# Kernel tuning notes

Hardware: AMD Instinct MI355X
Metric: run time of the kernel (lower is better)

## Reference

```python
import jax, jax.numpy as jnp
import numpy as np

N, E = 100000, 600000
DIN, DEMB, DOUT = 128, 128, 2
EPS = 1e-5


def setup_inputs() -> dict:
    key = jax.random.key(0)
    ks = jax.random.split(key, 20)
    s = 1.0 / np.sqrt(DIN)
    se = 1.0 / np.sqrt(DEMB)
    inp = {
        'x': jax.random.normal(ks[0], (N, DIN), jnp.float32),
        'edge_index': jax.random.randint(ks[1], (2, E), 0, N, jnp.int64),
        # SAGEConv layer 0 (in->emb): lin_l (with bias) on aggregated, lin_r (no bias) on root
        'Wl0': jax.random.uniform(ks[2], (DIN, DEMB), jnp.float32, -s, s),
        'bl0': jax.random.uniform(ks[3], (DEMB,), jnp.float32, -s, s),
        'Wr0': jax.random.uniform(ks[4], (DIN, DEMB), jnp.float32, -s, s),
        # SAGEConv layer 1 (emb->emb)
        'Wl1': jax.random.uniform(ks[5], (DEMB, DEMB), jnp.float32, -se, se),
        'bl1': jax.random.uniform(ks[6], (DEMB,), jnp.float32, -se, se),
        'Wr1': jax.random.uniform(ks[7], (DEMB, DEMB), jnp.float32, -se, se),
        # BatchNorm affine params (2 BN layers used)
        'g0': jnp.ones((DEMB,), jnp.float32),
        'be0': jnp.zeros((DEMB,), jnp.float32),
        'g1': jnp.ones((DEMB,), jnp.float32),
        'be1': jnp.zeros((DEMB,), jnp.float32),
        # MLP head
        'W1': jax.random.uniform(ks[8], (DEMB, DEMB), jnp.float32, -se, se),
        'b1': jax.random.uniform(ks[9], (DEMB,), jnp.float32, -se, se),
        'W2': jax.random.uniform(ks[10], (DEMB, DEMB), jnp.float32, -se, se),
        'b2': jax.random.uniform(ks[11], (DEMB,), jnp.float32, -se, se),
        'W3': jax.random.uniform(ks[12], (DEMB, DOUT), jnp.float32, -se, se),
        'b3': jax.random.uniform(ks[13], (DOUT,), jnp.float32, -se, se),
    }
    return inp


def _sage_conv(x, edge_index, Wl, bl, Wr):
    # sum-aggregate source features into destination nodes, then transform
    src, dst = edge_index[0], edge_index[1]
    agg = jax.ops.segment_sum(x[src], dst, num_segments=x.shape[0])  # [N, d]
    return agg @ Wl + bl + x @ Wr


def _bn_relu(h, gamma, beta):
    mu = jnp.mean(h, axis=0)
    var = jnp.var(h, axis=0)
    return jax.nn.relu((h - mu) * jax.lax.rsqrt(var + EPS) * gamma + beta)


def reference(x, edge_index, Wl0, bl0, Wr0, Wl1, bl1, Wr1,
              g0, be0, g1, be1, W1, b1, W2, b2, W3, b3):
    # NOTE: original forward zips num_layers convs with num_layers-1 batch_norms,
    # so only the first num_layers-1 = 2 conv blocks execute.
    h = _bn_relu(_sage_conv(x, edge_index, Wl0, bl0, Wr0), g0, be0)
    h = _bn_relu(_sage_conv(h, edge_index, Wl1, bl1, Wr1), g1, be1)
    # dropout p=0.2 is identity in inference mode
    h = jax.nn.relu(h @ W1 + b1)
    h = jax.nn.relu(h @ W2 + b2)
    return h @ W3 + b3
```

## Files before the change

### kernel.cpp

```cpp
#include <hip/hip_runtime.h>

#define EPS 1e-5f

typedef __attribute__((ext_vector_type(8))) short bf16x8;
typedef __attribute__((ext_vector_type(4))) float f32x4;

static __device__ __forceinline__ void split4(float4 f, ushort4& hi, ushort4& lo) {
    float v[4] = {f.x, f.y, f.z, f.w};
    ushort h[4], l[4];
#pragma unroll
    for (int i = 0; i < 4; ++i) {
        unsigned u = __float_as_uint(v[i]);
        h[i] = (ushort)(u >> 16);
        float r = v[i] - __uint_as_float(u & 0xffff0000u);
        l[i] = (ushort)(__float_as_uint(r) >> 16);
    }
    hi = make_ushort4(h[0], h[1], h[2], h[3]);
    lo = make_ushort4(l[0], l[1], l[2], l[3]);
}

static __device__ __forceinline__ float4 bnrelu4(float4 v, float4 a, float4 d) {
    float4 r;
    r.x = fmaxf(a.x * v.x + d.x, 0.f);
    r.y = fmaxf(a.y * v.y + d.y, 0.f);
    r.z = fmaxf(a.z * v.z + d.z, 0.f);
    r.w = fmaxf(a.w * v.w + d.w, 0.f);
    return r;
}

__global__ __launch_bounds__(256) void hist_kernel(
    const int* __restrict__ ei, int* __restrict__ deg, int E)
{
    int e = blockIdx.x * 256 + threadIdx.x;
    if (e >= E) return;
    atomicAdd(&deg[ei[E + e]], 1);
}

__global__ __launch_bounds__(256) void blocksum_kernel(
    const int* __restrict__ deg, int* __restrict__ bsum, int N)
{
    int i = blockIdx.x * 256 + threadIdx.x;
    int v = (i < N) ? deg[i] : 0;
#pragma unroll
    for (int o = 1; o < 64; o <<= 1) v += __shfl_xor(v, o);
    __shared__ int s[4];
    if ((threadIdx.x & 63) == 0) s[threadIdx.x >> 6] = v;
    __syncthreads();
    if (threadIdx.x == 0) bsum[blockIdx.x] = s[0] + s[1] + s[2] + s[3];
}

__global__ __launch_bounds__(512) void scanb_kernel(int* bsum, int NB)
{
    __shared__ int sh[512];
    int t = threadIdx.x;
    int v = (t < NB) ? bsum[t] : 0;
    sh[t] = v;
    __syncthreads();
    for (int o = 1; o < 512; o <<= 1) {
        int add = (t >= o) ? sh[t - o] : 0;
        __syncthreads();
        sh[t] += add;
        __syncthreads();
    }
    if (t < NB) bsum[t] = (t == 0) ? 0 : sh[t - 1];
}

__global__ __launch_bounds__(256) void scanfinal_kernel(
    const int* __restrict__ deg, const int* __restrict__ bsum,
    int* __restrict__ rowptr, int* __restrict__ cursor, int N)
{
    int b = blockIdx.x, t = threadIdx.x;
    int i = b * 256 + t;
    int v = (i < N) ? deg[i] : 0;
    __shared__ int sh[256];
    sh[t] = v;
    __syncthreads();
    for (int o = 1; o < 256; o <<= 1) {
        int add = (t >= o) ? sh[t - o] : 0;
        __syncthreads();
        sh[t] += add;
        __syncthreads();
    }
    int excl = sh[t] - v;
    if (i < N) {
        int rp = bsum[b] + excl;
        rowptr[i] = rp;
        cursor[i] = rp;
        if (i == N - 1) rowptr[N] = rp + v;
    }
}

__global__ __launch_bounds__(256) void fill_kernel(
    const int* __restrict__ ei, int* __restrict__ cursor, int* __restrict__ col, int E)
{
    int e = blockIdx.x * 256 + threadIdx.x;
    if (e >= E) return;
    int d = ei[E + e];
    int pos = atomicAdd(&cursor[d], 1);
    col[pos] = ei[e];
}

template<int BN>
__global__ __launch_bounds__(256) void gather_kernel(
    const float* __restrict__ feat, float* __restrict__ agg,
    const int* __restrict__ rowptr, const int* __restrict__ colIdx,
    const float* __restrict__ bnst, int N)
{
    int gid = blockIdx.x * 256 + threadIdx.x;
    int n = gid >> 5;
    if (n >= N) return;
    int l = gid & 31;
    float4 a4, d4;
    if (BN) {
        a4 = *(const float4*)(bnst + 256 + l * 4);
        d4 = *(const float4*)(bnst + 384 + l * 4);
    }
    int beg = rowptr[n], end = rowptr[n + 1];
    float ax = 0.f, ay = 0.f, az = 0.f, aw = 0.f;
    float bx = 0.f, by = 0.f, bz = 0.f, bw = 0.f;
    int e = beg;
    for (; e + 2 <= end; e += 2) {
        int s0 = colIdx[e], s1 = colIdx[e + 1];
        float4 v0 = *(const float4*)(feat + (size_t)s0 * 128 + l * 4);
        float4 v1 = *(const float4*)(feat + (size_t)s1 * 128 + l * 4);
        if (BN) { v0 = bnrelu4(v0, a4, d4); v1 = bnrelu4(v1, a4, d4); }
        ax += v0.x; ay += v0.y; az += v0.z; aw += v0.w;
        bx += v1.x; by += v1.y; bz += v1.z; bw += v1.w;
    }
    if (e < end) {
        int s0 = colIdx[e];
        float4 v0 = *(const float4*)(feat + (size_t)s0 * 128 + l * 4);
        if (BN) v0 = bnrelu4(v0, a4, d4);
        ax += v0.x; ay += v0.y; az += v0.z; aw += v0.w;
    }
    *(float4*)(agg + (size_t)n * 128 + l * 4) =
        make_float4(ax + bx, ay + by, az + bz, aw + bw);
}

__global__ __launch_bounds__(256) void prepack_kernel(
    const float* __restrict__ W0, const float* __restrict__ W1,
    const float* __restrict__ W2, const float* __restrict__ W3,
    const float* __restrict__ W4, const float* __restrict__ W5,
    ushort* __restrict__ wPk)
{
    int m = blockIdx.y;
    const float* W = (m == 0) ? W0 : (m == 1) ? W1 : (m == 2) ? W2
                   : (m == 3) ? W3 : (m == 4) ? W4 : W5;
    int base = m * 32768;
#pragma unroll
    for (int t = 0; t < 8; ++t) {
        int idx = blockIdx.x * 2048 + t * 256 + threadIdx.x;
        int j = idx & 7, l = (idx >> 3) & 63, cf = (idx >> 9) & 7, kb = idx >> 12;
        int k = kb * 32 + (l >> 4) * 8 + j;
        int n = cf * 16 + (l & 15);
        float v = W[k * 128 + n];
        unsigned u = __float_as_uint(v);
        wPk[base + idx] = (ushort)(u >> 16);
        float r = v - __uint_as_float(u & 0xffff0000u);
        wPk[base + 16384 + idx] = (ushort)(__float_as_uint(r) >> 16);
    }
}

template<int DUAL, int RELU, int STATS, int BN>
__global__ __launch_bounds__(512, 2) void plin_kernel(
    const float* __restrict__ Xa, const float* __restrict__ Xb,
    const ushort* __restrict__ wPair, const float* __restrict__ bias,
    const float* __restrict__ bnst, float* __restrict__ Y,
    float* __restrict__ stOut, int nrows)
{
    __shared__ ushort ldsA[(DUAL ? 2 : 1) * 2 * 2176];
    const int tid  = threadIdx.x;
    const int lane = tid & 63;
    const int w    = tid >> 6;
    const int q = lane >> 4, s = lane & 15;

    constexpr int NM = DUAL + 1;
    bf16x8 wf[NM][4][2];
#pragma unroll
    for (int m = 0; m < NM; ++m)
#pragma unroll
        for (int kb = 0; kb < 4; ++kb) {
            size_t o = (size_t)m * 32768 + (size_t)kb * 4096 + w * 512 + lane * 8;
            wf[m][kb][0] = *(const bf16x8*)(wPair + o);
            wf[m][kb][1] = *(const bf16x8*)(wPair + o + 16384);
        }

    const int srow  = tid >> 5;
    const int sunit = tid & 31;
    float4 bna, bnd;
    if (BN) {
        bna = *(const float4*)(bnst + 256 + sunit * 4);
        bnd = *(const float4*)(bnst + 384 + sunit * 4);
    }

    const int colc = w * 16 + s;
    const float bv = bias[colc];
    float cs = 0.f, cq = 0.f;

    const int NT = (nrows + 15) >> 4;
    const int stride = (int)gridDim.x;
    const int t0 = blockIdx.x;
    const int woff = srow * 136 + sunit * 4;

    if (t0 < NT) {
        int row = t0 * 16 + srow; if (row > nrows - 1) row = nrows - 1;
        float4 va = *(const float4*)(Xa + (size_t)row * 128 + sunit * 4);
        float4 vb;
        if (DUAL) vb = *(const float4*)(Xb + (size_t)row * 128 + sunit * 4);
        if (BN) { if (DUAL) vb = bnrelu4(vb, bna, bnd); else va = bnrelu4(va, bna, bnd); }
        ushort4 h, l;
        split4(va, h, l);
        *(ushort4*)(ldsA + woff)        = h;
        *(ushort4*)(ldsA + 2176 + woff) = l;
        if (DUAL) {
            split4(vb, h, l);
            *(ushort4*)(ldsA + 4352 + woff) = h;
            *(ushort4*)(ldsA + 6528 + woff) = l;
        }
    }

    for (int t = t0; t < NT; t += stride) {
        int tn = t + stride;
        float4 na, nb;
        if (tn < NT) {
            int row = tn * 16 + srow; if (row > nrows - 1) row = nrows - 1;
            na = *(const float4*)(Xa + (size_t)row * 128 + sunit * 4);
            if (DUAL) nb = *(const float4*)(Xb + (size_t)row * 128 + sunit * 4);
        }
        __syncthreads();

        f32x4 acc = (f32x4){0.f, 0.f, 0.f, 0.f};
#pragma unroll
        for (int m = 0; m < NM; ++m) {
            const ushort* pm = ldsA + m * 4352 + s * 136;
#pragma unroll
            for (int kb = 0; kb < 4; ++kb) {
                bf16x8 ah = *(const bf16x8*)(pm + (kb * 4 + q) * 8);
                bf16x8 al = *(const bf16x8*)(pm + 2176 + (kb * 4 + q) * 8);
                acc = __builtin_amdgcn_mfma_f32_16x16x32_bf16(ah, wf[m][kb][0], acc, 0, 0, 0);
                acc = __builtin_amdgcn_mfma_f32_16x16x32_bf16(al, wf[m][kb][0], acc, 0, 0, 0);
                acc = __builtin_amdgcn_mfma_f32_16x16x32_bf16(ah, wf[m][kb][1], acc, 0, 0, 0);
            }
        }

        int r0 = t * 16 + q * 4;
#pragma unroll
        for (int i = 0; i < 4; ++i) {
            int r = r0 + i;
            if (r < nrows) {
                float y = acc[i] + bv;
                if (RELU) y = fmaxf(y, 0.f);
                Y[(size_t)r * 128 + colc] = y;
                if (STATS) { cs += y; cq += y * y; }
            }
        }
        __syncthreads();
        if (tn < NT) {
            if (BN) { if (DUAL) nb = bnrelu4(nb, bna, bnd); else na = bnrelu4(na, bna, bnd); }
            ushort4 h, l;
            split4(na, h, l);
            *(ushort4*)(ldsA + woff)        = h;
            *(ushort4*)(ldsA + 2176 + woff) = l;
            if (DUAL) {
                split4(nb, h, l);
                *(ushort4*)(ldsA + 4352 + woff) = h;
                *(ushort4*)(ldsA + 6528 + woff) = l;
            }
        }
    }

    if (STATS) {
        cs += __shfl_xor(cs, 16); cs += __shfl_xor(cs, 32);
        cq += __shfl_xor(cq, 16); cq += __shfl_xor(cq, 32);
        if (q == 0) {
            atomicAdd(&stOut[colc], cs);
            atomicAdd(&stOut[128 + colc], cq);
        }
    }
}

__global__ void finalize_kernel(float* st, const float* __restrict__ g,
                                const float* __restrict__ be, float inv_n)
{
    int c = threadIdx.x;
    float mu = st[c] * inv_n;
    float var = st[128 + c] * inv_n - mu * mu;
    float rs = rsqrtf(var + EPS);
    float a = g[c] * rs;
    st[256 + c] = a;
    st[384 + c] = be[c] - mu * a;
}

__global__ __launch_bounds__(256) void linout_kernel(
    const float* __restrict__ X, const float* __restrict__ W, const float* __restrict__ b,
    float* __restrict__ out, int nrows)
{
    int r = blockIdx.x * 256 + threadIdx.x;
    if (r >= nrows) return;
    float a0 = 0.f, a1 = 0.f;
    const float* xr = X + (size_t)r * 128;
#pragma unroll 8
    for (int k = 0; k < 128; k += 4) {
        float4 x = *(const float4*)(xr + k);
        a0 += x.x * W[(k + 0) * 2]     + x.y * W[(k + 1) * 2]
            + x.z * W[(k + 2) * 2]     + x.w * W[(k + 3) * 2];
        a1 += x.x * W[(k + 0) * 2 + 1] + x.y * W[(k + 1) * 2 + 1]
            + x.z * W[(k + 2) * 2 + 1] + x.w * W[(k + 3) * 2 + 1];
    }
    float2 o = make_float2(a0 + b[0], a1 + b[1]);
    *(float2*)(out + (size_t)r * 2) = o;
}

extern "C" void kernel_launch(void* const* d_in, const int* in_sizes, int n_in,
                              void* d_out, int out_size, void* d_ws, size_t ws_size,
                              hipStream_t stream) {
    const float* x   = (const float*)d_in[0];
    const int*   ei  = (const int*)d_in[1];
    const float* Wl0 = (const float*)d_in[2];
    const float* bl0 = (const float*)d_in[3];
    const float* Wr0 = (const float*)d_in[4];
    const float* Wl1 = (const float*)d_in[5];
    const float* bl1 = (const float*)d_in[6];
    const float* Wr1 = (const float*)d_in[7];
    const float* g0  = (const float*)d_in[8];
    const float* be0 = (const float*)d_in[9];
    const float* g1  = (const float*)d_in[10];
    const float* be1 = (const float*)d_in[11];
    const float* W1  = (const float*)d_in[12];
    const float* b1  = (const float*)d_in[13];
    const float* W2  = (const float*)d_in[14];
    const float* b2  = (const float*)d_in[15];
    const float* W3  = (const float*)d_in[16];
    const float* b3  = (const float*)d_in[17];
    float* out = (float*)d_out;

    const int N = in_sizes[0] / 128;
    const int E = in_sizes[1] / 2;

    float* A   = (float*)d_ws;
    float* B   = A + (size_t)N * 128;
    float* st0 = B + (size_t)N * 128;
    float* st1 = st0 + 512;
    ushort* wPk = (ushort*)(st1 + 512);
    int* deg    = (int*)(wPk + 6 * 32768);
    int* rowptr = deg + N;
    int* cursor = rowptr + N + 1;
    int* col    = cursor + N;
    int* bsum   = col + E;

    const int edgeGrid   = (E + 255) / 256;
    const int nodeGrid   = (N + 255) / 256;
    const int gatherGrid = ((size_t)N * 32 + 255) / 256;
    const float inv_n = 1.0f / (float)N;

    prepack_kernel<<<dim3(8, 6), 256, 0, stream>>>(Wl0, Wr0, Wl1, Wr1, W1, W2, wPk);

    hipMemsetAsync(deg, 0, (size_t)N * sizeof(int), stream);
    hist_kernel<<<edgeGrid, 256, 0, stream>>>(ei, deg, E);
    blocksum_kernel<<<nodeGrid, 256, 0, stream>>>(deg, bsum, N);
    scanb_kernel<<<1, 512, 0, stream>>>(bsum, nodeGrid);
    scanfinal_kernel<<<nodeGrid, 256, 0, stream>>>(deg, bsum, rowptr, cursor, N);
    fill_kernel<<<edgeGrid, 256, 0, stream>>>(ei, cursor, col, E);

    gather_kernel<0><<<gatherGrid, 256, 0, stream>>>(x, A, rowptr, col, nullptr, N);
    hipMemsetAsync(st0, 0, 256 * sizeof(float), stream);
    plin_kernel<1, 0, 1, 0><<<512, 512, 0, stream>>>(
        A, x, wPk, bl0, nullptr, A, st0, N);
    finalize_kernel<<<1, 128, 0, stream>>>(st0, g0, be0, inv_n);

    gather_kernel<1><<<gatherGrid, 256, 0, stream>>>(A, B, rowptr, col, st0, N);
    hipMemsetAsync(st1, 0, 256 * sizeof(float), stream);
    plin_kernel<1, 0, 1, 1><<<512, 512, 0, stream>>>(
        B, A, wPk + 2 * 32768, bl1, st0, B, st1, N);
    finalize_kernel<<<1, 128, 0, stream>>>(st1, g1, be1, inv_n);

    plin_kernel<0, 1, 0, 1><<<512, 512, 0, stream>>>(
        B, nullptr, wPk + 4 * 32768, b1, st1, A, nullptr, N);
    plin_kernel<0, 1, 0, 0><<<512, 512, 0, stream>>>(
        A, nullptr, wPk + 5 * 32768, b2, nullptr, B, nullptr, N);
    linout_kernel<<<(N + 255) / 256, 256, 0, stream>>>(B, W3, b3, out, N);
}
```

Before: 299.3 us.

## Fuse neighbor gather into SAGE linear kernels and fuse MLP head into one kernel

The separate gather kernels are removed. Each SAGE layer now aggregates neighbor rows inside the MFMA linear kernel while staging a tile, so the aggregated matrix is never written to or read back from global memory. The three MLP-head layers (two 128x128 GEMMs plus the 128->2 output) become one kernel that keeps intermediates in LDS, which removes two full N x 128 round trips and two launches. In exchange, the irregular gather now sits on the GEMM kernel's critical path: it runs synchronously between tiles, and prefetch overlap is lost because the next tile is staged only after the barrier. Occupancy is fixed at 512 blocks of 512 threads.

```diff
diff --git a/kernel.cpp b/kernel.cpp
--- a/kernel.cpp
+++ b/kernel.cpp
@@ -98,43 +98,6 @@
     int d = ei[E + e];
     int pos = atomicAdd(&cursor[d], 1);
     col[pos] = ei[e];
-}
-
-template<int BN>
-__global__ __launch_bounds__(256) void gather_kernel(
-    const float* __restrict__ feat, float* __restrict__ agg,
-    const int* __restrict__ rowptr, const int* __restrict__ colIdx,
-    const float* __restrict__ bnst, int N)
-{
-    int gid = blockIdx.x * 256 + threadIdx.x;
-    int n = gid >> 5;
-    if (n >= N) return;
-    int l = gid & 31;
-    float4 a4, d4;
-    if (BN) {
-        a4 = *(const float4*)(bnst + 256 + l * 4);
-        d4 = *(const float4*)(bnst + 384 + l * 4);
-    }
-    int beg = rowptr[n], end = rowptr[n + 1];
-    float ax = 0.f, ay = 0.f, az = 0.f, aw = 0.f;
-    float bx = 0.f, by = 0.f, bz = 0.f, bw = 0.f;
-    int e = beg;
-    for (; e + 2 <= end; e += 2) {
-        int s0 = colIdx[e], s1 = colIdx[e + 1];
-        float4 v0 = *(const float4*)(feat + (size_t)s0 * 128 + l * 4);
-        float4 v1 = *(const float4*)(feat + (size_t)s1 * 128 + l * 4);
-        if (BN) { v0 = bnrelu4(v0, a4, d4); v1 = bnrelu4(v1, a4, d4); }
-        ax += v0.x; ay += v0.y; az += v0.z; aw += v0.w;
-        bx += v1.x; by += v1.y; bz += v1.z; bw += v1.w;
-    }
-    if (e < end) {
-        int s0 = colIdx[e];
-        float4 v0 = *(const float4*)(feat + (size_t)s0 * 128 + l * 4);
-        if (BN) v0 = bnrelu4(v0, a4, d4);
-        ax += v0.x; ay += v0.y; az += v0.z; aw += v0.w;
-    }
-    *(float4*)(agg + (size_t)n * 128 + l * 4) =
-        make_float4(ax + bx, ay + by, az + bz, aw + bw);
 }
 
 __global__ __launch_bounds__(256) void prepack_kernel(
@@ -161,23 +124,22 @@
     }
 }
 
-template<int DUAL, int RELU, int STATS, int BN>
-__global__ __launch_bounds__(512, 2) void plin_kernel(
-    const float* __restrict__ Xa, const float* __restrict__ Xb,
-    const ushort* __restrict__ wPair, const float* __restrict__ bias,
-    const float* __restrict__ bnst, float* __restrict__ Y,
-    float* __restrict__ stOut, int nrows)
-{
-    __shared__ ushort ldsA[(DUAL ? 2 : 1) * 2 * 2176];
+template<int BN>
+__global__ __launch_bounds__(512, 2) void glin_kernel(
+    const float* __restrict__ X, const int* __restrict__ rowptr,
+    const int* __restrict__ colIdx, const ushort* __restrict__ wPair,
+    const float* __restrict__ bias, const float* __restrict__ bnst,
+    float* __restrict__ Y, float* __restrict__ stOut, int nrows)
+{
+    __shared__ ushort ldsA[2 * 2 * 2176];
     const int tid  = threadIdx.x;
     const int lane = tid & 63;
     const int w    = tid >> 6;
     const int q = lane >> 4, s = lane & 15;
 
-    constexpr int NM = DUAL + 1;
-    bf16x8 wf[NM][4][2];
-#pragma unroll
-    for (int m = 0; m < NM; ++m)
+    bf16x8 wf[2][4][2];
+#pragma unroll
+    for (int m = 0; m < 2; ++m)
 #pragma unroll
         for (int kb = 0; kb < 4; ++kb) {
             size_t o = (size_t)m * 32768 + (size_t)kb * 4096 + w * 512 + lane * 8;
@@ -202,36 +164,46 @@
     const int t0 = blockIdx.x;
     const int woff = srow * 136 + sunit * 4;
 
-    if (t0 < NT) {
-        int row = t0 * 16 + srow; if (row > nrows - 1) row = nrows - 1;
-        float4 va = *(const float4*)(Xa + (size_t)row * 128 + sunit * 4);
-        float4 vb;
-        if (DUAL) vb = *(const float4*)(Xb + (size_t)row * 128 + sunit * 4);
-        if (BN) { if (DUAL) vb = bnrelu4(vb, bna, bnd); else va = bnrelu4(va, bna, bnd); }
+    auto stage = [&](int t) {
+        int row = t * 16 + srow; if (row > nrows - 1) row = nrows - 1;
+        float4 root = *(const float4*)(X + (size_t)row * 128 + sunit * 4);
+        int beg = rowptr[row], end = rowptr[row + 1];
+        float ax = 0.f, ay = 0.f, az = 0.f, aw = 0.f;
+        float bx = 0.f, by = 0.f, bz = 0.f, bw = 0.f;
+        int e = beg;
+        for (; e + 2 <= end; e += 2) {
+            int s0 = colIdx[e], s1 = colIdx[e + 1];
+            float4 v0 = *(const float4*)(X + (size_t)s0 * 128 + sunit * 4);
+            float4 v1 = *(const float4*)(X + (size_t)s1 * 128 + sunit * 4);
+            if (BN) { v0 = bnrelu4(v0, bna, bnd); v1 = bnrelu4(v1, bna, bnd); }
+            ax += v0.x; ay += v0.y; az += v0.z; aw += v0.w;
+            bx += v1.x; by += v1.y; bz += v1.z; bw += v1.w;
+        }
+        if (e < end) {
+            int s0 = colIdx[e];
+            float4 v0 = *(const float4*)(X + (size_t)s0 * 128 + sunit * 4);
+            if (BN) v0 = bnrelu4(v0, bna, bnd);
+            ax += v0.x; ay += v0.y; az += v0.z; aw += v0.w;
+        }
+        float4 agg = make_float4(ax + bx, ay + by, az + bz, aw + bw);
+        if (BN) root = bnrelu4(root, bna, bnd);
         ushort4 h, l;
-        split4(va, h, l);
+        split4(agg, h, l);
         *(ushort4*)(ldsA + woff)        = h;
         *(ushort4*)(ldsA + 2176 + woff) = l;
-        if (DUAL) {
-            split4(vb, h, l);
-            *(ushort4*)(ldsA + 4352 + woff) = h;
-            *(ushort4*)(ldsA + 6528 + woff) = l;
-        }
-    }
+        split4(root, h, l);
+        *(ushort4*)(ldsA + 4352 + woff) = h;
+        *(ushort4*)(ldsA + 6528 + woff) = l;
+    };
+
+    if (t0 < NT) stage(t0);
 
     for (int t = t0; t < NT; t += stride) {
-        int tn = t + stride;
-        float4 na, nb;
-        if (tn < NT) {
-            int row = tn * 16 + srow; if (row > nrows - 1) row = nrows - 1;
-            na = *(const float4*)(Xa + (size_t)row * 128 + sunit * 4);
-            if (DUAL) nb = *(const float4*)(Xb + (size_t)row * 128 + sunit * 4);
-        }
         __syncthreads();
 
         f32x4 acc = (f32x4){0.f, 0.f, 0.f, 0.f};
 #pragma unroll
-        for (int m = 0; m < NM; ++m) {
+        for (int m = 0; m < 2; ++m) {
             const ushort* pm = ldsA + m * 4352 + s * 136;
 #pragma unroll
             for (int kb = 0; kb < 4; ++kb) {
@@ -249,33 +221,134 @@
             int r = r0 + i;
             if (r < nrows) {
                 float y = acc[i] + bv;
-                if (RELU) y = fmaxf(y, 0.f);
                 Y[(size_t)r * 128 + colc] = y;
-                if (STATS) { cs += y; cq += y * y; }
+                cs += y; cq += y * y;
             }
         }
         __syncthreads();
-        if (tn < NT) {
-            if (BN) { if (DUAL) nb = bnrelu4(nb, bna, bnd); else na = bnrelu4(na, bna, bnd); }
+        int tn = t + stride;
+        if (tn < NT) stage(tn);
+    }
+
+    cs += __shfl_xor(cs, 16); cs += __shfl_xor(cs, 32);
+    cq += __shfl_xor(cq, 16); cq += __shfl_xor(cq, 32);
+    if (q == 0) {
+        atomicAdd(&stOut[colc], cs);
+        atomicAdd(&stOut[128 + colc], cq);
+    }
+}
+
+__global__ __launch_bounds__(512, 2) void mlp_kernel(
+    const float* __restrict__ X, const ushort* __restrict__ w1Pk,
+    const ushort* __restrict__ w2Pk, const float* __restrict__ b1,
+    const float* __restrict__ b2, const float* __restrict__ W3,
+    const float* __restrict__ b3, const float* __restrict__ bnst,
+    float* __restrict__ out, int nrows)
+{
+    __shared__ ushort ldsP[2 * 2176];
+    __shared__ float  ldsY[16 * 132];
+    const int tid  = threadIdx.x;
+    const int lane = tid & 63;
+    const int w    = tid >> 6;
+    const int q = lane >> 4, s = lane & 15;
+
+    bf16x8 wf1[4][2], wf2[4][2];
+#pragma unroll
+    for (int kb = 0; kb < 4; ++kb) {
+        size_t o = (size_t)kb * 4096 + w * 512 + lane * 8;
+        wf1[kb][0] = *(const bf16x8*)(w1Pk + o);
+        wf1[kb][1] = *(const bf16x8*)(w1Pk + o + 16384);
+        wf2[kb][0] = *(const bf16x8*)(w2Pk + o);
+        wf2[kb][1] = *(const bf16x8*)(w2Pk + o + 16384);
+    }
+
+    const int srow  = tid >> 5;
+    const int sunit = tid & 31;
+    float4 bna = *(const float4*)(bnst + 256 + sunit * 4);
+    float4 bnd = *(const float4*)(bnst + 384 + sunit * 4);
+
+    float w30[4], w31[4];
+#pragma unroll
+    for (int j = 0; j < 4; ++j) {
+        w30[j] = W3[(sunit * 4 + j) * 2];
+        w31[j] = W3[(sunit * 4 + j) * 2 + 1];
+    }
+    const float b30 = b3[0], b31 = b3[1];
+
+    const int colc = w * 16 + s;
+    const float bv1 = b1[colc];
+    const float bv2 = b2[colc];
+
+    const int NT = (nrows + 15) >> 4;
+    const int stride = (int)gridDim.x;
+    const int t0 = blockIdx.x;
+    const int woff = srow * 136 + sunit * 4;
+
+    auto stageX = [&](int t) {
+        int row = t * 16 + srow; if (row > nrows - 1) row = nrows - 1;
+        float4 v = *(const float4*)(X + (size_t)row * 128 + sunit * 4);
+        v = bnrelu4(v, bna, bnd);
+        ushort4 h, l;
+        split4(v, h, l);
+        *(ushort4*)(ldsP + woff)        = h;
+        *(ushort4*)(ldsP + 2176 + woff) = l;
+    };
+
+    auto gemm = [&](const bf16x8 (&wf)[4][2]) {
+        f32x4 acc = (f32x4){0.f, 0.f, 0.f, 0.f};
+        const ushort* pm = ldsP + s * 136;
+#pragma unroll
+        for (int kb = 0; kb < 4; ++kb) {
+            bf16x8 ah = *(const bf16x8*)(pm + (kb * 4 + q) * 8);
+            bf16x8 al = *(const bf16x8*)(pm + 2176 + (kb * 4 + q) * 8);
+            acc = __builtin_amdgcn_mfma_f32_16x16x32_bf16(ah, wf[kb][0], acc, 0, 0, 0);
+            acc = __builtin_amdgcn_mfma_f32_16x16x32_bf16(al, wf[kb][0], acc, 0, 0, 0);
+            acc = __builtin_amdgcn_mfma_f32_16x16x32_bf16(ah, wf[kb][1], acc, 0, 0, 0);
+        }
+        return acc;
+    };
+
+    if (t0 < NT) stageX(t0);
+
+    for (int t = t0; t < NT; t += stride) {
+        __syncthreads();
+
+        f32x4 acc = gemm(wf1);
+#pragma unroll
+        for (int i = 0; i < 4; ++i)
+            ldsY[(q * 4 + i) * 132 + colc] = fmaxf(acc[i] + bv1, 0.f);
+        __syncthreads();
+
+        {
+            float4 yv = *(const float4*)&ldsY[srow * 132 + sunit * 4];
             ushort4 h, l;
-            split4(na, h, l);
-            *(ushort4*)(ldsA + woff)        = h;
-            *(ushort4*)(ldsA + 2176 + woff) = l;
-            if (DUAL) {
-                split4(nb, h, l);
-                *(ushort4*)(ldsA + 4352 + woff) = h;
-                *(ushort4*)(ldsA + 6528 + woff) = l;
+            split4(yv, h, l);
+            *(ushort4*)(ldsP + woff)        = h;
+            *(ushort4*)(ldsP + 2176 + woff) = l;
+        }
+        __syncthreads();
+
+        acc = gemm(wf2);
+#pragma unroll
+        for (int i = 0; i < 4; ++i)
+            ldsY[(q * 4 + i) * 132 + colc] = fmaxf(acc[i] + bv2, 0.f);
+        __syncthreads();
+
+        {
+            float4 yv = *(const float4*)&ldsY[srow * 132 + sunit * 4];
+            float p0 = yv.x * w30[0] + yv.y * w30[1] + yv.z * w30[2] + yv.w * w30[3];
+            float p1 = yv.x * w31[0] + yv.y * w31[1] + yv.z * w31[2] + yv.w * w31[3];
+#pragma unroll
+            for (int o = 1; o < 32; o <<= 1) {
+                p0 += __shfl_xor(p0, o);
+                p1 += __shfl_xor(p1, o);
             }
-        }
-    }
-
-    if (STATS) {
-        cs += __shfl_xor(cs, 16); cs += __shfl_xor(cs, 32);
-        cq += __shfl_xor(cq, 16); cq += __shfl_xor(cq, 32);
-        if (q == 0) {
-            atomicAdd(&stOut[colc], cs);
-            atomicAdd(&stOut[128 + colc], cq);
-        }
+            int row = t * 16 + srow;
+            if (sunit == 0 && row < nrows)
+                *(float2*)(out + (size_t)row * 2) = make_float2(p0 + b30, p1 + b31);
+        }
+        int tn = t + stride;
+        if (tn < NT) stageX(tn);
     }
 }
 
@@ -289,26 +362,6 @@
     float a = g[c] * rs;
     st[256 + c] = a;
     st[384 + c] = be[c] - mu * a;
-}
-
-__global__ __launch_bounds__(256) void linout_kernel(
-    const float* __restrict__ X, const float* __restrict__ W, const float* __restrict__ b,
-    float* __restrict__ out, int nrows)
-{
-    int r = blockIdx.x * 256 + threadIdx.x;
-    if (r >= nrows) return;
-    float a0 = 0.f, a1 = 0.f;
-    const float* xr = X + (size_t)r * 128;
-#pragma unroll 8
-    for (int k = 0; k < 128; k += 4) {
-        float4 x = *(const float4*)(xr + k);
-        a0 += x.x * W[(k + 0) * 2]     + x.y * W[(k + 1) * 2]
-            + x.z * W[(k + 2) * 2]     + x.w * W[(k + 3) * 2];
-        a1 += x.x * W[(k + 0) * 2 + 1] + x.y * W[(k + 1) * 2 + 1]
-            + x.z * W[(k + 2) * 2 + 1] + x.w * W[(k + 3) * 2 + 1];
-    }
-    float2 o = make_float2(a0 + b[0], a1 + b[1]);
-    *(float2*)(out + (size_t)r * 2) = o;
 }
 
 extern "C" void kernel_launch(void* const* d_in, const int* in_sizes, int n_in,
@@ -348,9 +401,8 @@
     int* col    = cursor + N;
     int* bsum   = col + E;
 
-    const int edgeGrid   = (E + 255) / 256;
-    const int nodeGrid   = (N + 255) / 256;
-    const int gatherGrid = ((size_t)N * 32 + 255) / 256;
+    const int edgeGrid = (E + 255) / 256;
+    const int nodeGrid = (N + 255) / 256;
     const float inv_n = 1.0f / (float)N;
 
     prepack_kernel<<<dim3(8, 6), 256, 0, stream>>>(Wl0, Wr0, Wl1, Wr1, W1, W2, wPk);
@@ -362,21 +414,16 @@
     scanfinal_kernel<<<nodeGrid, 256, 0, stream>>>(deg, bsum, rowptr, cursor, N);
     fill_kernel<<<edgeGrid, 256, 0, stream>>>(ei, cursor, col, E);
 
-    gather_kernel<0><<<gatherGrid, 256, 0, stream>>>(x, A, rowptr, col, nullptr, N);
     hipMemsetAsync(st0, 0, 256 * sizeof(float), stream);
-    plin_kernel<1, 0, 1, 0><<<512, 512, 0, stream>>>(
-        A, x, wPk, bl0, nullptr, A, st0, N);
+    glin_kernel<0><<<512, 512, 0, stream>>>(
+        x, rowptr, col, wPk, bl0, nullptr, A, st0, N);
     finalize_kernel<<<1, 128, 0, stream>>>(st0, g0, be0, inv_n);
 
-    gather_kernel<1><<<gatherGrid, 256, 0, stream>>>(A, B, rowptr, col, st0, N);
     hipMemsetAsync(st1, 0, 256 * sizeof(float), stream);
-    plin_kernel<1, 0, 1, 1><<<512, 512, 0, stream>>>(
-        B, A, wPk + 2 * 32768, bl1, st0, B, st1, N);
+    glin_kernel<1><<<512, 512, 0, stream>>>(
+        A, rowptr, col, wPk + 2 * 32768, bl1, st0, B, st1, N);
     finalize_kernel<<<1, 128, 0, stream>>>(st1, g1, be1, inv_n);
 
-    plin_kernel<0, 1, 0, 1><<<512, 512, 0, stream>>>(
-        B, nullptr, wPk + 4 * 32768, b1, st1, A, nullptr, N);
-    plin_kernel<0, 1, 0, 0><<<512, 512, 0, stream>>>(
-        A, nullptr, wPk + 5 * 32768, b2, nullptr, B, nullptr, N);
-    linout_kernel<<<(N + 255) / 256, 256, 0, stream>>>(B, W3, b3, out, N);
-}
+    mlp_kernel<<<512, 512, 0, stream>>>(
+        B, wPk + 4 * 32768, wPk + 5 * 32768, b1, b2, W3, b3, st1, out, N);
+}
```

New measurement: 276.3 us. 7.7% less time.
